# Performance work log

Hardware: AMD Instinct MI355X
Metric: run time of the kernel (lower is better)

## Reference

```python
import jax, jax.numpy as jnp
import numpy as np

B, N, C, H, MLP = 4, 1024, 768, 6, 2304  # num_heads = C // 128
D = C // H  # head dim = 128


def setup_inputs() -> dict:
    key = jax.random.key(0)
    ks = iter(jax.random.split(key, 64))
    def nrm(shape, s=0.02):
        return jax.random.normal(next(ks), shape, jnp.float32) * s
    inp = {}
    for nm in ("queries", "change_emb", "imageA_emb", "imageB_emb", "pe"):
        inp[nm] = jax.random.normal(next(ks), (B, N, C), jnp.float32)
    # three Attention modules: self-attn (1), change->ABC cross (2), imageAB->change cross (3)
    for i in (1, 2, 3):
        for p in ("q", "k", "v", "o"):
            inp[f"w{p}{i}"] = nrm((C, C))       # stored [in, out]; y = x @ W + b
            inp[f"b{p}{i}"] = jnp.zeros((C,), jnp.float32)
    for i in (1, 2, 3):
        inp[f"ln{i}_w"] = jnp.ones((C,), jnp.float32)
        inp[f"ln{i}_b"] = jnp.zeros((C,), jnp.float32)
    inp["mlp_w1"] = nrm((C, MLP)); inp["mlp_b1"] = jnp.zeros((MLP,), jnp.float32)
    inp["mlp_w2"] = nrm((MLP, C)); inp["mlp_b2"] = jnp.zeros((C,), jnp.float32)
    inp["flag_a"] = nrm((C,)); inp["flag_b"] = nrm((C,)); inp["flag_c"] = nrm((C,))
    return inp


def _ln(x, w, b, eps=1e-5):
    m = jnp.mean(x, -1, keepdims=True)
    v = jnp.var(x, -1, keepdims=True)
    return (x - m) * jax.lax.rsqrt(v + eps) * w + b


def _mha(q, k, v, wq, bq, wk, bk, wv, bv, wo, bo):
    b, nq, _ = q.shape
    qh = (q @ wq + bq).reshape(b, nq, H, D)
    kh = (k @ wk + bk).reshape(b, k.shape[1], H, D)
    vh = (v @ wv + bv).reshape(b, v.shape[1], H, D)
    scores = jnp.einsum('bqhd,bkhd->bhqk', qh, kh) / np.float32(np.sqrt(D))
    attn = jax.nn.softmax(scores, axis=-1)
    out = jnp.einsum('bhqk,bkhd->bqhd', attn, vh).reshape(b, nq, H * D)
    return out @ wo + bo


def reference(queries, change_emb, imageA_emb, imageB_emb, pe,
              wq1, bq1, wk1, bk1, wv1, bv1, wo1, bo1,
              wq2, bq2, wk2, bk2, wv2, bv2, wo2, bo2,
              wq3, bq3, wk3, bk3, wv3, bv3, wo3, bo3,
              ln1_w, ln1_b, ln2_w, ln2_b, ln3_w, ln3_b,
              mlp_w1, mlp_b1, mlp_w2, mlp_b2,
              flag_a, flag_b, flag_c):
    # --- self attention on change queries (skip_first_layer_add=False) ---
    q0 = queries + change_emb
    a = _mha(q0 + pe, q0 + pe, q0, wq1, bq1, wk1, bk1, wv1, bv1, wo1, bo1)
    q1 = _ln(q0 + a, ln1_w, ln1_b)
    # --- cross attention: change -> [imageA, imageB, change] ---
    qf = q1 + pe + flag_c
    k2 = jnp.concatenate((imageA_emb + pe + flag_a,
                          imageB_emb + pe + flag_b,
                          q1 + pe + flag_c), axis=1)
    v2 = jnp.concatenate((imageA_emb, imageB_emb, q1), axis=1)
    a = _mha(qf, k2, v2, wq2, bq2, wk2, bk2, wv2, bv2, wo2, bo2)
    q2 = _ln(q1 + a, ln2_w, ln2_b)
    # --- MLP (exact GELU, as nn.GELU default) ---
    mlp_out = jax.nn.gelu(q2 @ mlp_w1 + mlp_b1, approximate=False) @ mlp_w2 + mlp_b2
    q3 = _ln(q2 + mlp_out, ln3_w, ln3_b)
    change_out = q3
    # --- cross attention: [imageA; imageB] -> [image; change], batched along dim 0 ---
    qa = imageA_emb + pe + flag_a
    qb = imageB_emb + pe + flag_b
    ka = jnp.concatenate((imageA_emb + pe + flag_a, q3 + pe + flag_c), axis=1)
    kb = jnp.concatenate((imageB_emb + pe + flag_b, q3 + pe + flag_c), axis=1)
    va = jnp.concatenate((imageA_emb, q3), axis=1)
    vb = jnp.concatenate((imageB_emb, q3), axis=1)
    q = jnp.concatenate((qa, qb), axis=0)   # [2B, N, C]
    k = jnp.concatenate((ka, kb), axis=0)   # [2B, 2N, C]
    v = jnp.concatenate((va, vb), axis=0)
    a = _mha(q, k, v, wq3, bq3, wk3, bk3, wv3, bv3, wo3, bo3)
    q = q + a
    image_A_refined, image_B_refined = jnp.split(q, 2, axis=0)
    return (image_A_refined, image_B_refined, change_out)
```

## Files before the change

kernel.cpp:

```cpp
#include <hip/hip_runtime.h>
#include <hip/hip_bf16.h>
#include <math.h>

typedef short bf16x8 __attribute__((ext_vector_type(8)));
typedef float f32x4 __attribute__((ext_vector_type(4)));
using bf16_t = __hip_bfloat16;

#define DEV static __device__ __forceinline__

DEV unsigned short f2bu(float x) {
  bf16_t h = __float2bfloat16(x);
  unsigned short u;
  __builtin_memcpy(&u, &h, 2);
  return u;
}
DEV void st4(bf16_t* p, float a, float b, float c, float d) {
  ushort4 u;
  u.x = f2bu(a); u.y = f2bu(b); u.z = f2bu(c); u.w = f2bu(d);
  *reinterpret_cast<ushort4*>(p) = u;
}

DEV int xcd_swz(int orig, int tot) {
  int q = tot >> 3, r = tot & 7;
  int xcd = orig & 7, pos = orig >> 3;
  int base = xcd < r ? xcd * (q + 1) : r * (q + 1) + (xcd - r) * q;
  return base + pos;
}

DEV void async_copy16(const bf16_t* g, bf16_t* lds) {
  __builtin_amdgcn_global_load_lds(
      (const __attribute__((address_space(1))) unsigned int*)g,
      (__attribute__((address_space(3))) unsigned int*)lds, 16, 0, 0);
}

struct WPack {
  const float* s[13];
  bf16_t* d[13];
  float scale[13];
};

__global__ __launch_bounds__(256) void k_wt13(WPack pk) {
  __shared__ float tile[32][33];
  int z = blockIdx.z;
  const float* W = pk.s[z];
  bf16_t* WT = pk.d[z];
  float scale = pk.scale[z];
  int i0 = blockIdx.x * 32;
  int o0 = blockIdx.y * 32;
  int tx = threadIdx.x & 31, ty = threadIdx.x >> 5;
  for (int r = ty; r < 32; r += 8)
    tile[r][tx] = W[(size_t)(i0 + r) * 768 + (o0 + tx)];
  __syncthreads();
  for (int r = ty; r < 32; r += 8)
    WT[(size_t)(o0 + r) * 768 + (i0 + tx)] = __float2bfloat16(tile[tx][r] * scale);
}

__global__ __launch_bounds__(256) void k_wt(const float* __restrict__ W, bf16_t* __restrict__ WT,
                                            int in_dim, int out_dim) {
  __shared__ float tile[32][33];
  int i0 = blockIdx.x * 32;
  int o0 = blockIdx.y * 32;
  int tx = threadIdx.x & 31, ty = threadIdx.x >> 5;
  for (int r = ty; r < 32; r += 8)
    tile[r][tx] = W[(size_t)(i0 + r) * out_dim + (o0 + tx)];
  __syncthreads();
  for (int r = ty; r < 32; r += 8)
    WT[(size_t)(o0 + r) * in_dim + (i0 + tx)] = __float2bfloat16(tile[tx][r]);
}

__global__ __launch_bounds__(256) void k_bcat(const float* __restrict__ s0, const float* __restrict__ s1,
                                              const float* __restrict__ s2, float a0,
                                              float* __restrict__ out, int nseg) {
  int i = blockIdx.x * 256 + threadIdx.x;
  if (i >= nseg * 768) return;
  int seg = i / 768, c = i - seg * 768;
  const float* s = seg == 0 ? s0 : (seg == 1 ? s1 : s2);
  out[i] = s[c] * (seg == 0 ? a0 : 1.0f);
}

__global__ __launch_bounds__(256) void k_prep1(const float4* __restrict__ q, const float4* __restrict__ ce,
                                               const float4* __restrict__ pe,
                                               bf16_t* __restrict__ qpe_b, bf16_t* __restrict__ q0_b, int n4) {
  int i = blockIdx.x * 256 + threadIdx.x;
  if (i >= n4) return;
  float4 a = q[i], b = ce[i], p = pe[i];
  float sx = a.x + b.x, sy = a.y + b.y, sz = a.z + b.z, sw = a.w + b.w;
  st4(q0_b + 4 * (size_t)i, sx, sy, sz, sw);
  st4(qpe_b + 4 * (size_t)i, sx + p.x, sy + p.y, sz + p.z, sw + p.w);
}

__global__ __launch_bounds__(256) void k_buildqq(const float* __restrict__ imA, const float* __restrict__ imB,
                                                 const float* __restrict__ pe, const float* __restrict__ fa,
                                                 const float* __restrict__ fb, bf16_t* __restrict__ qq,
                                                 bf16_t* __restrict__ imAB) {
  int idx = blockIdx.x * 256 + threadIdx.x;
  int c4 = idx % 192; int rem = idx / 192;
  int n = rem & 1023; int bb = rem >> 10;
  int b = bb & 3, isB = bb >> 2;
  int c = c4 * 4;
  size_t tok = (size_t)(b * 1024 + n) * 768 + c;
  float4 s = *(const float4*)((isB ? imB : imA) + tok);
  float4 p = *(const float4*)(pe + tok);
  float4 f = *(const float4*)((isB ? fb : fa) + c);
  size_t o = (size_t)rem * 768 + c;
  st4(imAB + o, s.x, s.y, s.z, s.w);
  st4(qq + o, s.x + p.x + f.x, s.y + p.y + f.y, s.z + p.z + f.z, s.w + p.w + f.w);
}

struct FArgs {
  const bf16_t* Q; bf16_t* O;
  const bf16_t* Kp[3]; const bf16_t* Vp[3];
  int badd[3], bmask[3];
  int ldq, ldk;
  long qStrideB, oStrideB;
};

template<int NSEG>
__global__ __launch_bounds__(256, 4) void k_flash(FArgs fa) {
  const int z = blockIdx.y; const int b = z / 6, h = z % 6;
  const bf16_t* Qb = fa.Q + (size_t)b * fa.qStrideB + h * 128;
  bf16_t* Ob = fa.O + (size_t)b * fa.oStrideB + h * 128;
  const int q0 = blockIdx.x * 64;
  const int tid = threadIdx.x, lane = tid & 63, w = tid >> 6;
  const int g = lane >> 4, c = lane & 15;

  __shared__ bf16_t Ks[64][136];
  __shared__ bf16_t Vs[128][72];
  bf16_t* Ps = &Ks[0][0];

  bf16x8 qf[4];
#pragma unroll
  for (int kk = 0; kk < 4; kk++)
    qf[kk] = *reinterpret_cast<const bf16x8*>(
        &Qb[(size_t)(q0 + w * 16 + c) * fa.ldq + kk * 32 + g * 8]);

  f32x4 oa[8];
  float m[4], l[4];
#pragma unroll
  for (int d = 0; d < 8; d++) { f32x4 zz = {0.f, 0.f, 0.f, 0.f}; oa[d] = zz; }
#pragma unroll
  for (int r = 0; r < 4; r++) { m[r] = -1.0e30f; l[r] = 0.f; }

  const int kr_ = tid >> 4, kc_ = (tid & 15) * 8;
  const int vr_ = tid >> 3, vc_ = (tid & 7) * 8;
  const int ldk = fa.ldk;

#pragma unroll
  for (int s = 0; s < NSEG; ++s) {
    const int bi = fa.badd[s] + (b & fa.bmask[s]);
    const bf16_t* Kb = fa.Kp[s] + (size_t)bi * 1024 * ldk + h * 128;
    const bf16_t* Vb = fa.Vp[s] + (size_t)(bi * 6 + h) * 128 * 1024;
    for (int t = 0; t < 16; ++t) {
      const int k0 = t << 6;
#pragma unroll
      for (int p = 0; p < 4; p++)
        *reinterpret_cast<uint4*>(&Ks[p * 16 + kr_][kc_]) =
            *reinterpret_cast<const uint4*>(&Kb[(size_t)(k0 + p * 16 + kr_) * ldk + kc_]);
#pragma unroll
      for (int p = 0; p < 4; p++)
        *reinterpret_cast<uint4*>(&Vs[p * 32 + vr_][vc_]) =
            *reinterpret_cast<const uint4*>(&Vb[(size_t)(p * 32 + vr_) * 1024 + k0 + vc_]);
      __syncthreads();

      f32x4 sx[4];
#pragma unroll
      for (int j = 0; j < 4; j++) { f32x4 zz = {0.f, 0.f, 0.f, 0.f}; sx[j] = zz; }
      __builtin_amdgcn_s_setprio(1);
#pragma unroll
      for (int kk = 0; kk < 4; kk++)
#pragma unroll
        for (int j = 0; j < 4; j++) {
          bf16x8 kf = *reinterpret_cast<const bf16x8*>(&Ks[j * 16 + c][kk * 32 + g * 8]);
          sx[j] = __builtin_amdgcn_mfma_f32_16x16x32_bf16(qf[kk], kf, sx[j], 0, 0, 0);
        }
      __builtin_amdgcn_s_setprio(0);

      float tl[4];
#pragma unroll
      for (int r = 0; r < 4; r++)
        tl[r] = fmaxf(fmaxf(sx[0][r], sx[1][r]), fmaxf(sx[2][r], sx[3][r]));
      float ex = fmaxf(fmaxf(tl[0] - m[0], tl[1] - m[1]), fmaxf(tl[2] - m[2], tl[3] - m[3]));
      if (__any(ex > 8.0f)) {
#pragma unroll
        for (int r = 0; r < 4; r++) {
          float tv = tl[r];
          tv = fmaxf(tv, __shfl_xor(tv, 1));
          tv = fmaxf(tv, __shfl_xor(tv, 2));
          tv = fmaxf(tv, __shfl_xor(tv, 4));
          tv = fmaxf(tv, __shfl_xor(tv, 8));
          float mn = fmaxf(m[r], tv);
          float f = exp2f(m[r] - mn);
          m[r] = mn;
          l[r] *= f;
#pragma unroll
          for (int d = 0; d < 8; d++) oa[d][r] *= f;
        }
      }

      __syncthreads();

#pragma unroll
      for (int j = 0; j < 4; j++)
#pragma unroll
        for (int r = 0; r < 4; r++) {
          float p = exp2f(sx[j][r] - m[r]);
          l[r] += p;
          Ps[(w * 16 + g * 4 + r) * 72 + j * 16 + c] = __float2bfloat16(p);
        }

      __builtin_amdgcn_s_setprio(1);
#pragma unroll
      for (int kk = 0; kk < 2; kk++) {
        bf16x8 pf = *reinterpret_cast<const bf16x8*>(&Ps[(w * 16 + c) * 72 + kk * 32 + g * 8]);
#pragma unroll
        for (int d = 0; d < 8; d++) {
          bf16x8 vf = *reinterpret_cast<const bf16x8*>(&Vs[d * 16 + c][kk * 32 + g * 8]);
          oa[d] = __builtin_amdgcn_mfma_f32_16x16x32_bf16(pf, vf, oa[d], 0, 0, 0);
        }
      }
      __builtin_amdgcn_s_setprio(0);
      __syncthreads();
    }
  }

  float inv[4];
#pragma unroll
  for (int r = 0; r < 4; r++) {
    float t2 = l[r];
    t2 += __shfl_xor(t2, 1);
    t2 += __shfl_xor(t2, 2);
    t2 += __shfl_xor(t2, 4);
    t2 += __shfl_xor(t2, 8);
    inv[r] = 1.0f / t2;
  }
#pragma unroll
  for (int d = 0; d < 8; d++) {
    int col = d * 16 + c;
#pragma unroll
    for (int r = 0; r < 4; r++) {
      int row = q0 + w * 16 + g * 4 + r;
      Ob[(size_t)row * 768 + col] = __float2bfloat16(oa[d][r] * inv[r]);
    }
  }
}

__global__ __launch_bounds__(256) void k_ln(const float* __restrict__ X1, const float* __restrict__ X2,
                                            const float* __restrict__ A,
                                            const float* __restrict__ w, const float* __restrict__ bvec,
                                            float* __restrict__ outf, bf16_t* __restrict__ outb,
                                            const float* __restrict__ pe, const float* __restrict__ flag,
                                            bf16_t* __restrict__ outpf) {
  int row = blockIdx.x, tid = threadIdx.x;
  size_t base = (size_t)row * 768;
  float v0 = X1[base + tid] + A[base + tid];
  float v1 = X1[base + tid + 256] + A[base + tid + 256];
  float v2 = X1[base + tid + 512] + A[base + tid + 512];
  if (X2) {
    v0 += X2[base + tid]; v1 += X2[base + tid + 256]; v2 += X2[base + tid + 512];
  }
  float s = v0 + v1 + v2;
  for (int o = 32; o; o >>= 1) s += __shfl_xor(s, o);
  __shared__ float sm[8];
  int wv = tid >> 6, ln = tid & 63;
  if (ln == 0) sm[wv] = s;
  __syncthreads();
  s = sm[0] + sm[1] + sm[2] + sm[3];
  float mean = s * (1.0f / 768.0f);
  float d0 = v0 - mean, d1 = v1 - mean, d2 = v2 - mean;
  float ss = d0 * d0 + d1 * d1 + d2 * d2;
  for (int o = 32; o; o >>= 1) ss += __shfl_xor(ss, o);
  if (ln == 0) sm[4 + wv] = ss;
  __syncthreads();
  ss = sm[4] + sm[5] + sm[6] + sm[7];
  float rstd = rsqrtf(ss * (1.0f / 768.0f) + 1e-5f);
  float o0 = d0 * rstd * w[tid] + bvec[tid];
  float o1 = d1 * rstd * w[tid + 256] + bvec[tid + 256];
  float o2 = d2 * rstd * w[tid + 512] + bvec[tid + 512];
  outf[base + tid] = o0; outf[base + tid + 256] = o1; outf[base + tid + 512] = o2;
  if (outb) {
    outb[base + tid] = __float2bfloat16(o0);
    outb[base + tid + 256] = __float2bfloat16(o1);
    outb[base + tid + 512] = __float2bfloat16(o2);
  }
  if (outpf) {
    outpf[base + tid] = __float2bfloat16(o0 + pe[base + tid] + flag[tid]);
    outpf[base + tid + 256] = __float2bfloat16(o1 + pe[base + tid + 256] + flag[tid + 256]);
    outpf[base + tid + 512] = __float2bfloat16(o2 + pe[base + tid + 512] + flag[tid + 512]);
  }
}

struct GArgs {
  const bf16_t* X; const bf16_t* Wt; const float* bias;
  void* O0; void* O1; void* O2;
  const bf16_t* resid;
  int K, ldx, ldw, ldo, vNk, mode;
};
struct GPack {
  GArgs a[7];
  int cum[7];
  int nx[7];
  int tot;
};

__global__ __launch_bounds__(256, 2) void k_gemmN(GPack pk) {
  GArgs a; int gbase, nx;
  int sidx = xcd_swz(blockIdx.x, pk.tot);
  {
    int idx = sidx;
    if (idx < pk.cum[0])      { a = pk.a[0]; gbase = 0;          nx = pk.nx[0]; }
    else if (idx < pk.cum[1]) { a = pk.a[1]; gbase = pk.cum[0];  nx = pk.nx[1]; }
    else if (idx < pk.cum[2]) { a = pk.a[2]; gbase = pk.cum[1];  nx = pk.nx[2]; }
    else if (idx < pk.cum[3]) { a = pk.a[3]; gbase = pk.cum[2];  nx = pk.nx[3]; }
    else if (idx < pk.cum[4]) { a = pk.a[4]; gbase = pk.cum[3];  nx = pk.nx[4]; }
    else if (idx < pk.cum[5]) { a = pk.a[5]; gbase = pk.cum[4];  nx = pk.nx[5]; }
    else                      { a = pk.a[6]; gbase = pk.cum[5];  nx = pk.nx[6]; }
  }
  int idx = sidx - gbase;
  const int brow = (idx / nx) * 128;
  const int bcol = (idx % nx) * 128;

  __shared__ bf16_t As[128 * 32];
  __shared__ bf16_t Bs[128 * 32];

  const int tid = threadIdx.x;
  const int lane = tid & 63;
  const int wave = tid >> 6;
  const int wr = wave >> 1;
  const int wc = wave & 1;

  f32x4 acc[4][4];
#pragma unroll
  for (int i = 0; i < 4; i++)
#pragma unroll
    for (int j = 0; j < 4; j++) {
      f32x4 zz = {0.f, 0.f, 0.f, 0.f};
      acc[i][j] = zz;
    }

  const int sr = lane >> 2;
  const int sc = (lane & 3) * 8;
  const int lrow = lane & 15;
  const int kch = (lane >> 4) * 8;

  const int nK = a.K >> 5;
  for (int kk = 0; kk < nK; ++kk) {
    const int k0 = kk << 5;
#pragma unroll
    for (int q = 0; q < 2; q++) {
      const int rows = wave * 32 + q * 16;
      async_copy16(a.X + (size_t)(brow + rows + sr) * a.ldx + k0 + sc, As + rows * 32);
      async_copy16(a.Wt + (size_t)(bcol + rows + sr) * a.ldw + k0 + sc, Bs + rows * 32);
    }
    __syncthreads();

    bf16x8 afr[4], bfr[4];
#pragma unroll
    for (int i = 0; i < 4; i++)
      afr[i] = *reinterpret_cast<const bf16x8*>(&As[(wr * 64 + i * 16 + lrow) * 32 + kch]);
#pragma unroll
    for (int j = 0; j < 4; j++)
      bfr[j] = *reinterpret_cast<const bf16x8*>(&Bs[(wc * 64 + j * 16 + lrow) * 32 + kch]);
#pragma unroll
    for (int i = 0; i < 4; i++)
#pragma unroll
      for (int j = 0; j < 4; j++)
        acc[i][j] = __builtin_amdgcn_mfma_f32_16x16x32_bf16(afr[i], bfr[j], acc[i][j], 0, 0, 0);
    __syncthreads();
  }

  const int lcol = lane & 15;
  const int lrow4 = (lane >> 4) * 4;

  int seg = 0;
  if (a.O1) seg = bcol / 768;
  void* ob = seg == 0 ? a.O0 : (seg == 1 ? a.O1 : a.O2);
  const int cofs = seg * 768;

  if (a.mode == 2) {
    const int bi = brow / a.vNk;
    const int n0 = brow - bi * a.vNk;
#pragma unroll
    for (int i = 0; i < 4; i++) {
      int rloc = n0 + wr * 64 + i * 16 + lrow4;
#pragma unroll
      for (int j = 0; j < 4; j++) {
        int colf = bcol + wc * 64 + j * 16 + lcol;
        int col = colf - cofs;
        int hh = col >> 7, dd = col & 127;
        float bv = a.bias[colf];
        ushort4 u;
        u.x = f2bu(acc[i][j][0] + bv);
        u.y = f2bu(acc[i][j][1] + bv);
        u.z = f2bu(acc[i][j][2] + bv);
        u.w = f2bu(acc[i][j][3] + bv);
        bf16_t* dst = reinterpret_cast<bf16_t*>(ob) +
                      ((size_t)(bi * 6 + hh) * 128 + dd) * (size_t)a.vNk + rloc;
        *reinterpret_cast<ushort4*>(dst) = u;
      }
    }
  } else if (a.mode == 3) {
#pragma unroll
    for (int i = 0; i < 4; i++) {
      int row0 = brow + wr * 64 + i * 16 + lrow4;
#pragma unroll
      for (int j = 0; j < 4; j++) {
        int col = bcol + wc * 64 + j * 16 + lcol;
        float bv = a.bias[col];
#pragma unroll
        for (int r = 0; r < 4; r++) {
          size_t idx2 = (size_t)(row0 + r) * a.ldo + col;
          float rv = __bfloat162float(a.resid[(size_t)(row0 + r) * 768 + col]);
          reinterpret_cast<float*>(a.O0)[idx2] = acc[i][j][r] + bv + rv;
        }
      }
    }
  } else {
#pragma unroll
    for (int i = 0; i < 4; i++) {
      int row0 = brow + wr * 64 + i * 16 + lrow4;
#pragma unroll
      for (int j = 0; j < 4; j++) {
        int colf = bcol + wc * 64 + j * 16 + lcol;
        int col = colf - cofs;
        float bv = a.bias[colf];
#pragma unroll
        for (int r = 0; r < 4; r++)
          reinterpret_cast<bf16_t*>(ob)[(size_t)(row0 + r) * a.ldo + col] =
              __float2bfloat16(acc[i][j][r] + bv);
      }
    }
  }
}

static inline void packN(hipStream_t st, const GArgs* as, const int* Ms, const int* Ns, int n) {
  GPack pk;
  int tot = 0;
  for (int i = 0; i < 7; ++i) {
    int j = i < n ? i : n - 1;
    pk.a[i] = as[j];
    pk.nx[i] = Ns[j] / 128;
    if (i < n) tot += (Ns[j] / 128) * (Ms[j] / 128);
    pk.cum[i] = tot;
  }
  pk.tot = tot;
  k_gemmN<<<dim3(tot), 256, 0, st>>>(pk);
}

template<int OUTBF, int GELU>
__global__ __launch_bounds__(256, 2) void k_gemm(
    const bf16_t* __restrict__ X, const bf16_t* __restrict__ Wt,
    const float* __restrict__ bias, void* __restrict__ Out,
    int M, int Nout, int K, int ldx, int ldw, int ldo, float alpha) {
  int tot = gridDim.x * gridDim.y;
  int lin = blockIdx.y * gridDim.x + blockIdx.x;
  int sidx = xcd_swz(lin, tot);
  const int brow = (sidx / gridDim.x) * 128;
  const int bcol = (sidx % gridDim.x) * 128;

  __shared__ bf16_t As[128 * 32];
  __shared__ bf16_t Bs[128 * 32];

  const int tid = threadIdx.x;
  const int lane = tid & 63;
  const int wave = tid >> 6;
  const int wr = wave >> 1;
  const int wc = wave & 1;

  f32x4 acc[4][4];
#pragma unroll
  for (int i = 0; i < 4; i++)
#pragma unroll
    for (int j = 0; j < 4; j++) {
      f32x4 zz = {0.f, 0.f, 0.f, 0.f};
      acc[i][j] = zz;
    }

  const int sr = lane >> 2;
  const int sc = (lane & 3) * 8;
  const int lrow = lane & 15;
  const int kch = (lane >> 4) * 8;

  const int nK = K >> 5;
  for (int kk = 0; kk < nK; ++kk) {
    const int k0 = kk << 5;
#pragma unroll
    for (int q = 0; q < 2; q++) {
      const int rows = wave * 32 + q * 16;
      async_copy16(X + (size_t)(brow + rows + sr) * ldx + k0 + sc, As + rows * 32);
      async_copy16(Wt + (size_t)(bcol + rows + sr) * ldw + k0 + sc, Bs + rows * 32);
    }
    __syncthreads();

    bf16x8 afr[4], bfr[4];
#pragma unroll
    for (int i = 0; i < 4; i++)
      afr[i] = *reinterpret_cast<const bf16x8*>(&As[(wr * 64 + i * 16 + lrow) * 32 + kch]);
#pragma unroll
    for (int j = 0; j < 4; j++)
      bfr[j] = *reinterpret_cast<const bf16x8*>(&Bs[(wc * 64 + j * 16 + lrow) * 32 + kch]);
#pragma unroll
    for (int i = 0; i < 4; i++)
#pragma unroll
      for (int j = 0; j < 4; j++)
        acc[i][j] = __builtin_amdgcn_mfma_f32_16x16x32_bf16(afr[i], bfr[j], acc[i][j], 0, 0, 0);
    __syncthreads();
  }

  const int lcol = lane & 15;
  const int lrow4 = (lane >> 4) * 4;

#pragma unroll
  for (int i = 0; i < 4; i++) {
    int row0 = brow + wr * 64 + i * 16 + lrow4;
#pragma unroll
    for (int j = 0; j < 4; j++) {
      int col = bcol + wc * 64 + j * 16 + lcol;
      float bv = bias ? bias[col] : 0.0f;
#pragma unroll
      for (int r = 0; r < 4; r++) {
        float v = (acc[i][j][r] + bv) * alpha;
        if (GELU) v = 0.5f * v * (1.0f + erff(v * 0.70710678118f));
        size_t idx = (size_t)(row0 + r) * ldo + col;
        if (OUTBF) reinterpret_cast<bf16_t*>(Out)[idx] = __float2bfloat16(v);
        else reinterpret_cast<float*>(Out)[idx] = v;
      }
    }
  }
}

static inline void gemm(hipStream_t st, const bf16_t* X, const bf16_t* Wt, const float* bias,
                        void* out, int outBf, int gelu, int M, int N, int K,
                        int ldx, int ldw, int ldo, float alpha = 1.0f) {
  dim3 g(N / 128, M / 128), blk(256);
  if (outBf) {
    if (gelu) k_gemm<1, 1><<<g, blk, 0, st>>>(X, Wt, bias, out, M, N, K, ldx, ldw, ldo, alpha);
    else      k_gemm<1, 0><<<g, blk, 0, st>>>(X, Wt, bias, out, M, N, K, ldx, ldw, ldo, alpha);
  } else      k_gemm<0, 0><<<g, blk, 0, st>>>(X, Wt, bias, out, M, N, K, ldx, ldw, ldo, alpha);
}

extern "C" void kernel_launch(void* const* d_in, const int* in_sizes, int n_in,
                              void* d_out, int out_size, void* d_ws, size_t ws_size,
                              hipStream_t stream) {
  (void)in_sizes; (void)n_in; (void)out_size; (void)ws_size;
  constexpr int B = 4, N = 1024, C = 768, Hh = 6, MLPD = 2304;
  constexpr size_t BNC = (size_t)B * N * C;
  constexpr size_t NC  = (size_t)N * C;
  const float qalpha = 0.08838834764831845f * 1.4426950408889634f;

  const float* queries = (const float*)d_in[0];
  const float* change  = (const float*)d_in[1];
  const float* imA     = (const float*)d_in[2];
  const float* imB     = (const float*)d_in[3];
  const float* pe      = (const float*)d_in[4];
  const float* bq1 = (const float*)d_in[6];  const float* bk1 = (const float*)d_in[8];
  const float* bv1 = (const float*)d_in[10]; const float* bo1 = (const float*)d_in[12];
  const float* bq2 = (const float*)d_in[14]; const float* bk2 = (const float*)d_in[16];
  const float* bv2 = (const float*)d_in[18]; const float* bo2 = (const float*)d_in[20];
  const float* bq3 = (const float*)d_in[22]; const float* bk3 = (const float*)d_in[24];
  const float* bv3 = (const float*)d_in[26]; const float* bo3 = (const float*)d_in[28];
  const float* ln1w = (const float*)d_in[29]; const float* ln1b = (const float*)d_in[30];
  const float* ln2w = (const float*)d_in[31]; const float* ln2b = (const float*)d_in[32];
  const float* ln3w = (const float*)d_in[33]; const float* ln3b = (const float*)d_in[34];
  const float* mb1 = (const float*)d_in[36]; const float* mb2 = (const float*)d_in[38];
  const float* fa = (const float*)d_in[39];
  const float* fb = (const float*)d_in[40];
  const float* fc = (const float*)d_in[41];

  char* base = (char*)d_ws;
  size_t off = 0;
  auto alloc = [&](size_t bytes) -> void* {
    void* p = base + off;
    off += (bytes + 255) & ~(size_t)255;
    return p;
  };

  bf16_t* WT[12]; bf16_t* WT5b; bf16_t* WTm1; bf16_t* WTm2;
  WT[0] = (bf16_t*)alloc((size_t)768 * 768 * 2);
  WT[1] = (bf16_t*)alloc((size_t)768 * 768 * 2);
  WT[2] = (bf16_t*)alloc((size_t)768 * 768 * 2);
  WT[3] = (bf16_t*)alloc((size_t)768 * 768 * 2);
  WT[8] = (bf16_t*)alloc((size_t)768 * 768 * 2);
  WT[5] = (bf16_t*)alloc((size_t)768 * 768 * 2);
  WT[9] = (bf16_t*)alloc((size_t)768 * 768 * 2);
  WT[6] = (bf16_t*)alloc((size_t)768 * 768 * 2);
  WT[10] = (bf16_t*)alloc((size_t)768 * 768 * 2);
  WT[4] = (bf16_t*)alloc((size_t)768 * 768 * 2);
  WT5b  = (bf16_t*)alloc((size_t)768 * 768 * 2);
  WT[7] = (bf16_t*)alloc((size_t)768 * 768 * 2);
  WT[11] = (bf16_t*)alloc((size_t)768 * 768 * 2);
  WTm1 = (bf16_t*)alloc((size_t)768 * 2304 * 2);
  WTm2 = (bf16_t*)alloc((size_t)2304 * 768 * 2);
  float* bqk1  = (float*)alloc(1536 * 4);
  float* bKm   = (float*)alloc(2304 * 4);
  float* bVm   = (float*)alloc(1536 * 4);
  float* bQ2K2 = (float*)alloc(1536 * 4);
  float*  q1  = (float*)alloc(BNC * 4);
  float*  q2  = (float*)alloc(BNC * 4);
  bf16_t* q2b = (bf16_t*)alloc(BNC * 2);
  bf16_t* q1b = (bf16_t*)alloc(BNC * 2);
  bf16_t* qf  = (bf16_t*)alloc(BNC * 2);
  bf16_t* qq   = (bf16_t*)alloc(2 * BNC * 2);
  bf16_t* Q3h  = (bf16_t*)alloc(2 * BNC * 2);
  bf16_t* K2i  = (bf16_t*)alloc(2 * BNC * 2);
  bf16_t* vT2i = (bf16_t*)alloc(2 * BNC * 2);
  bf16_t* K3i  = (bf16_t*)alloc(2 * BNC * 2);
  bf16_t* vT3i = (bf16_t*)alloc(2 * BNC * 2);
  const size_t arena = off;

  float* dof = (float*)d_out;
  float* chg = dof + 2 * BNC;

  {
    WPack pk;
    const int widx[12] = {5, 7, 9, 11, 13, 15, 17, 19, 21, 23, 25, 27};
    for (int i = 0; i < 12; i++) {
      pk.s[i] = (const float*)d_in[widx[i]];
      pk.d[i] = WT[i];
      pk.scale[i] = (i == 0 || i == 4 || i == 8) ? qalpha : 1.0f;
    }
    pk.s[12] = (const float*)d_in[15]; pk.d[12] = WT5b; pk.scale[12] = 1.0f;
    k_wt13<<<dim3(24, 24, 13), 256, 0, stream>>>(pk);
  }
  k_wt<<<dim3(24, 72), 256, 0, stream>>>((const float*)d_in[35], WTm1, 768, 2304);
  k_wt<<<dim3(72, 24), 256, 0, stream>>>((const float*)d_in[37], WTm2, 2304, 768);
  k_bcat<<<dim3(6), 256, 0, stream>>>(bq1, bk1, nullptr, qalpha, bqk1, 2);
  k_bcat<<<dim3(9), 256, 0, stream>>>(bq3, bk2, bk3, qalpha, bKm, 3);
  k_bcat<<<dim3(6), 256, 0, stream>>>(bv2, bv3, nullptr, 1.0f, bVm, 2);
  k_bcat<<<dim3(6), 256, 0, stream>>>(bq2, bk2, nullptr, qalpha, bQ2K2, 2);

  off = arena;
  bf16_t* qpe_b = (bf16_t*)alloc(BNC * 2);
  bf16_t* q0_b  = (bf16_t*)alloc(BNC * 2);
  bf16_t* imAB  = (bf16_t*)alloc(2 * BNC * 2);
  bf16_t* QKh   = (bf16_t*)alloc((size_t)B * N * 1536 * 2);
  bf16_t* vT1   = (bf16_t*)alloc(BNC * 2);
  bf16_t* attC  = (bf16_t*)alloc(BNC * 2);
  float*  a1    = dof;

  k_prep1<<<dim3((int)(BNC / 4 / 256)), 256, 0, stream>>>(
      (const float4*)queries, (const float4*)change, (const float4*)pe, qpe_b, q0_b, (int)(BNC / 4));
  k_buildqq<<<dim3((int)(2 * BNC / 4 / 256)), 256, 0, stream>>>(imA, imB, pe, fa, fb, qq, imAB);
  {
    GArgs as[4] = {
      {qpe_b, WT[0], bqk1, QKh,  nullptr, nullptr, nullptr, C, C, C, 1536, 0,    1},
      {q0_b,  WT[2], bv1,  vT1,  nullptr, nullptr, nullptr, C, C, C, 0,    1024, 2},
      {qq,    WT[8], bKm,  Q3h,  K2i,     K3i,     nullptr, C, C, C, 768,  0,    1},
      {imAB,  WT[6], bVm,  vT2i, vT3i,    nullptr, nullptr, C, C, C, 0,    1024, 2},
    };
    int Ms[4] = {B * N, B * N, 2 * B * N, 2 * B * N};
    int Ns[4] = {1536, C, 2304, 1536};
    packN(stream, as, Ms, Ns, 4);
  }
  {
    FArgs f1 = {QKh, attC, {QKh + 768, QKh + 768, QKh + 768}, {vT1, vT1, vT1},
                {0, 0, 0}, {7, 7, 7}, 1536, 1536, (long)N * 1536, (long)NC};
    k_flash<1><<<dim3(16, B * Hh), 256, 0, stream>>>(f1);
  }
  gemm(stream, attC, WT[3], bo1, a1, 0, 0, B * N, C, C, C, C, C);
  k_ln<<<dim3(B * N), 256, 0, stream>>>(queries, change, a1, ln1w, ln1b, q1, q1b, pe, fc, qf);

  off = arena;
  bf16_t* Q2h   = (bf16_t*)alloc(BNC * 2);
  bf16_t* K2c   = (bf16_t*)alloc(BNC * 2);
  bf16_t* vT2c  = (bf16_t*)alloc(BNC * 2);
  bf16_t* attC2 = (bf16_t*)alloc(BNC * 2);
  float*  a2    = dof;

  {
    GArgs as[2] = {
      {qf,  WT[4], bQ2K2, Q2h,  K2c,    nullptr, nullptr, C, C, C, 768,  0,    1},
      {q1b, WT[6], bv2,   vT2c, nullptr, nullptr, nullptr, C, C, C, 0,    1024, 2},
    };
    int Ms[2] = {B * N, B * N};
    int Ns[2] = {1536, C};
    packN(stream, as, Ms, Ns, 2);
  }
  {
    FArgs f2 = {Q2h, attC2, {K2i, K2i, K2c}, {vT2i, vT2i, vT2c},
                {0, 4, 0}, {3, 3, 3}, C, C, (long)NC, (long)NC};
    k_flash<3><<<dim3(16, B * Hh), 256, 0, stream>>>(f2);
  }
  gemm(stream, attC2, WT[7], bo2, a2, 0, 0, B * N, C, C, C, C, C);
  k_ln<<<dim3(B * N), 256, 0, stream>>>(q1, (const float*)nullptr, a2, ln2w, ln2b, q2, q2b,
                                        (const float*)nullptr, (const float*)nullptr, (bf16_t*)nullptr);

  off = arena;
  bf16_t* h1 = (bf16_t*)alloc((size_t)B * N * MLPD * 2);
  float*  a3 = dof;
  gemm(stream, q2b, WTm1, mb1, h1, 1, 1, B * N, MLPD, C, C, C, MLPD);
  gemm(stream, h1, WTm2, mb2, a3, 0, 0, B * N, C, MLPD, MLPD, MLPD, C);

  off = arena;
  bf16_t* cf    = (bf16_t*)alloc(BNC * 2);
  bf16_t* chgb  = (bf16_t*)alloc(BNC * 2);
  bf16_t* K3c   = (bf16_t*)alloc(BNC * 2);
  bf16_t* vT3c  = (bf16_t*)alloc(BNC * 2);
  bf16_t* attC3 = (bf16_t*)alloc(2 * BNC * 2);

  k_ln<<<dim3(B * N), 256, 0, stream>>>(q2, (const float*)nullptr, a3, ln3w, ln3b, chg, chgb,
                                        pe, fc, cf);
  {
    GArgs as[2] = {
      {cf,   WT[9],  bk3, K3c,  nullptr, nullptr, nullptr, C, C, C, 768,  0,    1},
      {chgb, WT[10], bv3, vT3c, nullptr, nullptr, nullptr, C, C, C, 0,    1024, 2},
    };
    int Ms[2] = {B * N, B * N};
    int Ns[2] = {C, C};
    packN(stream, as, Ms, Ns, 2);
  }
  {
    FArgs f3 = {Q3h, attC3, {K3i, K3c, K3c}, {vT3i, vT3c, vT3c},
                {0, 0, 0}, {7, 3, 3}, C, C, (long)NC, (long)NC};
    k_flash<2><<<dim3(16, 2 * B * Hh), 256, 0, stream>>>(f3);
  }
  {
    GArgs as[1] = {{attC3, WT[11], bo3, dof, nullptr, nullptr, qq, C, C, C, C, 0, 3}};
    int Ms[1] = {2 * B * N};
    int Ns[1] = {C};
    packN(stream, as, Ms, Ns, 1);
  }
}
```

Baseline: 636.5 us.

## Warp-specialize flash attention into QK/softmax producers and PV consumer waves

```diff
diff --git a/kernel.cpp b/kernel.cpp
--- a/kernel.cpp
+++ b/kernel.cpp
@@ -116,52 +116,85 @@
 };
 
 template<int NSEG>
-__global__ __launch_bounds__(256, 4) void k_flash(FArgs fa) {
+__global__ __launch_bounds__(512, 4) void k_flash(FArgs fa) {
   const int z = blockIdx.y; const int b = z / 6, h = z % 6;
   const bf16_t* Qb = fa.Q + (size_t)b * fa.qStrideB + h * 128;
   bf16_t* Ob = fa.O + (size_t)b * fa.oStrideB + h * 128;
   const int q0 = blockIdx.x * 64;
   const int tid = threadIdx.x, lane = tid & 63, w = tid >> 6;
   const int g = lane >> 4, c = lane & 15;
+  const bool prod = w < 4;
+  const int wq = w & 3;
 
   __shared__ bf16_t Ks[64][136];
-  __shared__ bf16_t Vs[128][72];
-  bf16_t* Ps = &Ks[0][0];
-
-  bf16x8 qf[4];
-#pragma unroll
-  for (int kk = 0; kk < 4; kk++)
-    qf[kk] = *reinterpret_cast<const bf16x8*>(
-        &Qb[(size_t)(q0 + w * 16 + c) * fa.ldq + kk * 32 + g * 8]);
-
-  f32x4 oa[8];
-  float m[4], l[4];
-#pragma unroll
-  for (int d = 0; d < 8; d++) { f32x4 zz = {0.f, 0.f, 0.f, 0.f}; oa[d] = zz; }
-#pragma unroll
-  for (int r = 0; r < 4; r++) { m[r] = -1.0e30f; l[r] = 0.f; }
+  __shared__ bf16_t Vs[2][128][72];
+  __shared__ bf16_t Ps[2][64][72];
+  __shared__ float Fl[2][64];
+  __shared__ float Ls[64];
+
+  const int ldk = fa.ldk;
+  const int NT = NSEG * 16;
 
   const int kr_ = tid >> 4, kc_ = (tid & 15) * 8;
   const int vr_ = tid >> 3, vc_ = (tid & 7) * 8;
-  const int ldk = fa.ldk;
-
-#pragma unroll
-  for (int s = 0; s < NSEG; ++s) {
-    const int bi = fa.badd[s] + (b & fa.bmask[s]);
+
+  auto loadK = [&](int t, uint4* rg) {
+    int s = t >> 4;
+    int bi = fa.badd[s] + (b & fa.bmask[s]);
     const bf16_t* Kb = fa.Kp[s] + (size_t)bi * 1024 * ldk + h * 128;
+    int k0 = (t & 15) << 6;
+#pragma unroll
+    for (int p = 0; p < 2; p++)
+      rg[p] = *reinterpret_cast<const uint4*>(&Kb[(size_t)(k0 + p * 32 + kr_) * ldk + kc_]);
+  };
+  auto writeK = [&](uint4* rg) {
+#pragma unroll
+    for (int p = 0; p < 2; p++)
+      *reinterpret_cast<uint4*>(&Ks[p * 32 + kr_][kc_]) = rg[p];
+  };
+  auto loadV = [&](int t, uint4* rg) {
+    int s = t >> 4;
+    int bi = fa.badd[s] + (b & fa.bmask[s]);
     const bf16_t* Vb = fa.Vp[s] + (size_t)(bi * 6 + h) * 128 * 1024;
-    for (int t = 0; t < 16; ++t) {
-      const int k0 = t << 6;
-#pragma unroll
-      for (int p = 0; p < 4; p++)
-        *reinterpret_cast<uint4*>(&Ks[p * 16 + kr_][kc_]) =
-            *reinterpret_cast<const uint4*>(&Kb[(size_t)(k0 + p * 16 + kr_) * ldk + kc_]);
-#pragma unroll
-      for (int p = 0; p < 4; p++)
-        *reinterpret_cast<uint4*>(&Vs[p * 32 + vr_][vc_]) =
-            *reinterpret_cast<const uint4*>(&Vb[(size_t)(p * 32 + vr_) * 1024 + k0 + vc_]);
-      __syncthreads();
-
+    int k0 = (t & 15) << 6;
+#pragma unroll
+    for (int p = 0; p < 2; p++)
+      rg[p] = *reinterpret_cast<const uint4*>(&Vb[(size_t)(p * 64 + vr_) * 1024 + k0 + vc_]);
+  };
+  auto writeV = [&](int t, uint4* rg) {
+#pragma unroll
+    for (int p = 0; p < 2; p++)
+      *reinterpret_cast<uint4*>(&Vs[t & 1][p * 64 + vr_][vc_]) = rg[p];
+  };
+
+  bf16x8 qf[4];
+  float m[4], l[4];
+  f32x4 oa[8];
+  if (prod) {
+#pragma unroll
+    for (int kk = 0; kk < 4; kk++)
+      qf[kk] = *reinterpret_cast<const bf16x8*>(
+          &Qb[(size_t)(q0 + wq * 16 + c) * fa.ldq + kk * 32 + g * 8]);
+#pragma unroll
+    for (int r = 0; r < 4; r++) { m[r] = -1.0e30f; l[r] = 0.f; }
+  } else {
+#pragma unroll
+    for (int d = 0; d < 8; d++) { f32x4 zz = {0.f, 0.f, 0.f, 0.f}; oa[d] = zz; }
+  }
+
+  {
+    uint4 k0r[2], v0r[2];
+    loadK(0, k0r); loadV(0, v0r);
+    writeK(k0r); writeV(0, v0r);
+  }
+  __syncthreads();
+
+  uint4 kreg[2], vreg[2];
+  for (int t = 0; t < NT; ++t) {
+    const bool pre = (t + 1 < NT);
+    if (pre) { loadK(t + 1, kreg); loadV(t + 1, vreg); }
+
+    if (prod) {
       f32x4 sx[4];
 #pragma unroll
       for (int j = 0; j < 4; j++) { f32x4 zz = {0.f, 0.f, 0.f, 0.f}; sx[j] = zz; }
@@ -179,6 +212,7 @@
 #pragma unroll
       for (int r = 0; r < 4; r++)
         tl[r] = fmaxf(fmaxf(sx[0][r], sx[1][r]), fmaxf(sx[2][r], sx[3][r]));
+      float f_[4] = {1.f, 1.f, 1.f, 1.f};
       float ex = fmaxf(fmaxf(tl[0] - m[0], tl[1] - m[1]), fmaxf(tl[2] - m[2], tl[3] - m[3]));
       if (__any(ex > 8.0f)) {
 #pragma unroll
@@ -189,57 +223,93 @@
           tv = fmaxf(tv, __shfl_xor(tv, 4));
           tv = fmaxf(tv, __shfl_xor(tv, 8));
           float mn = fmaxf(m[r], tv);
-          float f = exp2f(m[r] - mn);
+          f_[r] = exp2f(m[r] - mn);
           m[r] = mn;
-          l[r] *= f;
-#pragma unroll
-          for (int d = 0; d < 8; d++) oa[d][r] *= f;
+          l[r] *= f_[r];
         }
       }
-
-      __syncthreads();
-
 #pragma unroll
       for (int j = 0; j < 4; j++)
 #pragma unroll
         for (int r = 0; r < 4; r++) {
           float p = exp2f(sx[j][r] - m[r]);
           l[r] += p;
-          Ps[(w * 16 + g * 4 + r) * 72 + j * 16 + c] = __float2bfloat16(p);
+          Ps[t & 1][wq * 16 + g * 4 + r][j * 16 + c] = __float2bfloat16(p);
         }
-
+      if (c == 0) {
+#pragma unroll
+        for (int r = 0; r < 4; r++) Fl[t & 1][wq * 16 + g * 4 + r] = f_[r];
+      }
+    } else if (t > 0) {
+      const int pb = (t - 1) & 1;
+#pragma unroll
+      for (int r = 0; r < 4; r++) {
+        float fr = Fl[pb][wq * 16 + g * 4 + r];
+#pragma unroll
+        for (int d = 0; d < 8; d++) oa[d][r] *= fr;
+      }
       __builtin_amdgcn_s_setprio(1);
 #pragma unroll
       for (int kk = 0; kk < 2; kk++) {
-        bf16x8 pf = *reinterpret_cast<const bf16x8*>(&Ps[(w * 16 + c) * 72 + kk * 32 + g * 8]);
+        bf16x8 pf = *reinterpret_cast<const bf16x8*>(&Ps[pb][wq * 16 + c][kk * 32 + g * 8]);
 #pragma unroll
         for (int d = 0; d < 8; d++) {
-          bf16x8 vf = *reinterpret_cast<const bf16x8*>(&Vs[d * 16 + c][kk * 32 + g * 8]);
+          bf16x8 vf = *reinterpret_cast<const bf16x8*>(&Vs[pb][d * 16 + c][kk * 32 + g * 8]);
           oa[d] = __builtin_amdgcn_mfma_f32_16x16x32_bf16(pf, vf, oa[d], 0, 0, 0);
         }
       }
       __builtin_amdgcn_s_setprio(0);
-      __syncthreads();
-    }
-  }
-
-  float inv[4];
-#pragma unroll
-  for (int r = 0; r < 4; r++) {
-    float t2 = l[r];
-    t2 += __shfl_xor(t2, 1);
-    t2 += __shfl_xor(t2, 2);
-    t2 += __shfl_xor(t2, 4);
-    t2 += __shfl_xor(t2, 8);
-    inv[r] = 1.0f / t2;
-  }
-#pragma unroll
-  for (int d = 0; d < 8; d++) {
-    int col = d * 16 + c;
-#pragma unroll
-    for (int r = 0; r < 4; r++) {
-      int row = q0 + w * 16 + g * 4 + r;
-      Ob[(size_t)row * 768 + col] = __float2bfloat16(oa[d][r] * inv[r]);
+    }
+    __syncthreads();
+
+    if (pre) { writeK(kreg); writeV(t + 1, vreg); }
+    __syncthreads();
+  }
+
+  {
+    const int pb = (NT - 1) & 1;
+    if (prod) {
+#pragma unroll
+      for (int r = 0; r < 4; r++) {
+        float t2 = l[r];
+        t2 += __shfl_xor(t2, 1);
+        t2 += __shfl_xor(t2, 2);
+        t2 += __shfl_xor(t2, 4);
+        t2 += __shfl_xor(t2, 8);
+        if (c == 0) Ls[wq * 16 + g * 4 + r] = t2;
+      }
+    } else {
+#pragma unroll
+      for (int r = 0; r < 4; r++) {
+        float fr = Fl[pb][wq * 16 + g * 4 + r];
+#pragma unroll
+        for (int d = 0; d < 8; d++) oa[d][r] *= fr;
+      }
+#pragma unroll
+      for (int kk = 0; kk < 2; kk++) {
+        bf16x8 pf = *reinterpret_cast<const bf16x8*>(&Ps[pb][wq * 16 + c][kk * 32 + g * 8]);
+#pragma unroll
+        for (int d = 0; d < 8; d++) {
+          bf16x8 vf = *reinterpret_cast<const bf16x8*>(&Vs[pb][d * 16 + c][kk * 32 + g * 8]);
+          oa[d] = __builtin_amdgcn_mfma_f32_16x16x32_bf16(pf, vf, oa[d], 0, 0, 0);
+        }
+      }
+    }
+  }
+  __syncthreads();
+
+  if (!prod) {
+    float inv[4];
+#pragma unroll
+    for (int r = 0; r < 4; r++) inv[r] = 1.0f / Ls[wq * 16 + g * 4 + r];
+#pragma unroll
+    for (int d = 0; d < 8; d++) {
+      int col = d * 16 + c;
+#pragma unroll
+      for (int r = 0; r < 4; r++) {
+        int row = q0 + wq * 16 + g * 4 + r;
+        Ob[(size_t)row * 768 + col] = __float2bfloat16(oa[d][r] * inv[r]);
+      }
     }
   }
 }
@@ -654,7 +724,7 @@
   {
     FArgs f1 = {QKh, attC, {QKh + 768, QKh + 768, QKh + 768}, {vT1, vT1, vT1},
                 {0, 0, 0}, {7, 7, 7}, 1536, 1536, (long)N * 1536, (long)NC};
-    k_flash<1><<<dim3(16, B * Hh), 256, 0, stream>>>(f1);
+    k_flash<1><<<dim3(16, B * Hh), 512, 0, stream>>>(f1);
   }
   gemm(stream, attC, WT[3], bo1, a1, 0, 0, B * N, C, C, C, C, C);
   k_ln<<<dim3(B * N), 256, 0, stream>>>(queries, change, a1, ln1w, ln1b, q1, q1b, pe, fc, qf);
@@ -678,7 +748,7 @@
   {
     FArgs f2 = {Q2h, attC2, {K2i, K2i, K2c}, {vT2i, vT2i, vT2c},
                 {0, 4, 0}, {3, 3, 3}, C, C, (long)NC, (long)NC};
-    k_flash<3><<<dim3(16, B * Hh), 256, 0, stream>>>(f2);
+    k_flash<3><<<dim3(16, B * Hh), 512, 0, stream>>>(f2);
   }
   gemm(stream, attC2, WT[7], bo2, a2, 0, 0, B * N, C, C, C, C, C);
   k_ln<<<dim3(B * N), 256, 0, stream>>>(q1, (const float*)nullptr, a2, ln2w, ln2b, q2, q2b,
@@ -711,7 +781,7 @@
   {
     FArgs f3 = {Q3h, attC3, {K3i, K3c, K3c}, {vT3i, vT3c, vT3c},
                 {0, 0, 0}, {7, 3, 3}, C, C, (long)NC, (long)NC};
-    k_flash<2><<<dim3(16, 2 * B * Hh), 256, 0, stream>>>(f3);
+    k_flash<2><<<dim3(16, 2 * B * Hh), 512, 0, stream>>>(f3);
   }
   {
     GArgs as[1] = {{attC3, WT[11], bo3, dof, nullptr, nullptr, qq, C, C, C, C, 0, 3}};
```

Result: slower. 957.2 us (+50.4%).
